# Optimization experiments

Measured on AMD Instinct MI355X. Metric: run time of the kernel, lower is better.

The kernel has to match this reference:

```python
import jax, jax.numpy as jnp
import numpy as np

WEIGHT = 0.1
NEIGHBORHOOD_SIZE = 3
EPSILON = 1e-06


def setup_inputs() -> dict:
    key = jax.random.key(0)
    x = jax.random.normal(key, (8, 3, 1024, 1024), dtype=jnp.float32)
    return {"x": x}


def reference(x):
    b, c, h, w = x.shape
    total = jnp.zeros((), dtype=x.dtype)
    for k in range(-NEIGHBORHOOD_SIZE, NEIGHBORHOOD_SIZE + 1):
        for l in range(-NEIGHBORHOOD_SIZE, NEIGHBORHOOD_SIZE + 1):
            if k == 0 and l == 0:
                continue
            shifted = jnp.roll(x, shift=(k, l), axis=(2, 3))
            diff = jnp.abs(x - shifted)
            total = total + jnp.sqrt(diff * diff + EPSILON).sum()
    return WEIGHT * total / (b * c * h * w)
```

## Files before the change

### kernel.cpp

```cpp
#include <hip/hip_runtime.h>


#define HDIM 1024
#define WDIM 1024
#define PLANES 24
#define MASK 1023
#define NTOT (PLANES * HDIM * WDIM)
#define RROWS 16
#define BLOCKS_PER_PLANE (HDIM / RROWS)
#define NBLOCKS (PLANES * BLOCKS_PER_PLANE)

__device__ __forceinline__ void load_row(const float* __restrict__ rb,
                                         int j, int cl, int cr, float* w) {
    float4 a = *(const float4*)(rb + cl);
    float4 b = *(const float4*)(rb + j);
    float4 c = *(const float4*)(rb + cr);
    w[0] = a.x; w[1] = a.y; w[2]  = a.z; w[3]  = a.w;
    w[4] = b.x; w[5] = b.y; w[6]  = b.z; w[7]  = b.w;
    w[8] = c.x; w[9] = c.y; w[10] = c.z; w[11] = c.w;
}

__global__ __launch_bounds__(256) void btv_main(const float* __restrict__ x,
                                                float* __restrict__ partial) {
    const int plane  = blockIdx.x / BLOCKS_PER_PLANE;
    const int istart = (blockIdx.x % BLOCKS_PER_PLANE) * RROWS;
    const int j  = threadIdx.x << 2;
    const int cl = (j - 4) & MASK;
    const int cr = (j + 4) & MASK;
    const float* pbase = x + (size_t)plane * (HDIM * WDIM);

    float buf[RROWS + 3][12];

#pragma unroll
    for (int m = 0; m < 6; ++m)
        load_row(pbase + (((istart + m) & MASK) * WDIM), j, cl, cr, buf[m]);

    float acc0 = 0.f, acc1 = 0.f, acc2 = 0.f, acc3 = 0.f;

#pragma unroll
    for (int r = 0; r < RROWS; ++r) {
        if (r + 6 <= RROWS + 2)
            load_row(pbase + (((istart + r + 6) & MASK) * WDIM), j, cl, cr,
                     buf[r + 6]);

        const float* w0 = buf[r];
        const float* w1 = buf[r + 1];
        const float* w2 = buf[r + 2];
        const float* w3 = buf[r + 3];

#pragma unroll
        for (int p = 0; p < 4; ++p) {
            const float own = w0[4 + p];
            float a = 0.f;
            a += fabsf(own - w0[5 + p]);
            a += fabsf(own - w0[6 + p]);
            a += fabsf(own - w0[7 + p]);
#pragma unroll
            for (int l = -3; l <= 3; ++l) a += fabsf(own - w1[4 + p + l]);
#pragma unroll
            for (int l = -3; l <= 3; ++l) a += fabsf(own - w2[4 + p + l]);
#pragma unroll
            for (int l = -3; l <= 3; ++l) a += fabsf(own - w3[4 + p + l]);
            if (p == 0) acc0 += a;
            else if (p == 1) acc1 += a;
            else if (p == 2) acc2 += a;
            else acc3 += a;
        }
    }

    float acc = (acc0 + acc1) + (acc2 + acc3);

#pragma unroll
    for (int off = 32; off > 0; off >>= 1)
        acc += __shfl_down(acc, off, 64);

    __shared__ float s[4];
    const int lane = threadIdx.x & 63;
    const int wid  = threadIdx.x >> 6;
    if (lane == 0) s[wid] = acc;
    __syncthreads();
    if (threadIdx.x == 0)
        partial[blockIdx.x] = (s[0] + s[1]) + (s[2] + s[3]);
}

__global__ __launch_bounds__(256) void btv_fin(const float* __restrict__ partial,
                                               float* __restrict__ out) {
    double s = 0.0;
    for (int i = threadIdx.x; i < NBLOCKS; i += 256)
        s += (double)partial[i];
#pragma unroll
    for (int off = 32; off > 0; off >>= 1)
        s += __shfl_down(s, off, 64);
    __shared__ double sh[4];
    const int lane = threadIdx.x & 63;
    const int wid  = threadIdx.x >> 6;
    if (lane == 0) sh[wid] = s;
    __syncthreads();
    if (threadIdx.x == 0) {
        double t = (sh[0] + sh[1]) + (sh[2] + sh[3]);
        *out = (float)(t * (0.2 / (double)NTOT));
    }
}

extern "C" void kernel_launch(void* const* d_in, const int* in_sizes, int n_in,
                              void* d_out, int out_size, void* d_ws, size_t ws_size,
                              hipStream_t stream) {
    const float* x = (const float*)d_in[0];
    float* out = (float*)d_out;
    float* partial = (float*)d_ws;

    btv_main<<<NBLOCKS, 256, 0, stream>>>(x, partial);
    btv_fin<<<1, 256, 0, stream>>>(partial, out);
}
```

Before: 150.6 us.

## Use rolling 8-slot register ring buffer with 32 rows per block

Replaces the fully unrolled per-block row buffer with an 8-slot circular register buffer of float4 rows. This allows 32 rows per block, halving the redundant halo row reloads, and adds a launch-bounds occupancy hint. Loads of the next row are issued one iteration ahead inside a partially unrolled outer loop. It halves the block count and may add register pressure or reduce the prefetch distance compared to the earlier six-row lookahead.

```diff
diff --git a/kernel.cpp b/kernel.cpp
--- a/kernel.cpp
+++ b/kernel.cpp
@@ -6,22 +6,16 @@
 #define PLANES 24
 #define MASK 1023
 #define NTOT (PLANES * HDIM * WDIM)
-#define RROWS 16
+#define RROWS 32
 #define BLOCKS_PER_PLANE (HDIM / RROWS)
 #define NBLOCKS (PLANES * BLOCKS_PER_PLANE)
 
-__device__ __forceinline__ void load_row(const float* __restrict__ rb,
-                                         int j, int cl, int cr, float* w) {
-    float4 a = *(const float4*)(rb + cl);
-    float4 b = *(const float4*)(rb + j);
-    float4 c = *(const float4*)(rb + cr);
-    w[0] = a.x; w[1] = a.y; w[2]  = a.z; w[3]  = a.w;
-    w[4] = b.x; w[5] = b.y; w[6]  = b.z; w[7]  = b.w;
-    w[8] = c.x; w[9] = c.y; w[10] = c.z; w[11] = c.w;
+__device__ __forceinline__ float getc(const float4 v, int c) {
+    return c == 0 ? v.x : (c == 1 ? v.y : (c == 2 ? v.z : v.w));
 }
 
-__global__ __launch_bounds__(256) void btv_main(const float* __restrict__ x,
-                                                float* __restrict__ partial) {
+__global__ __launch_bounds__(256, 3) void btv_main(const float* __restrict__ x,
+                                                   float* __restrict__ partial) {
     const int plane  = blockIdx.x / BLOCKS_PER_PLANE;
     const int istart = (blockIdx.x % BLOCKS_PER_PLANE) * RROWS;
     const int j  = threadIdx.x << 2;
@@ -29,55 +23,69 @@
     const int cr = (j + 4) & MASK;
     const float* pbase = x + (size_t)plane * (HDIM * WDIM);
 
-    float buf[RROWS + 3][12];
+    float4 buf[8][3];
+
+#define LOAD_ROW(slot, m) do {                                          \
+        const float* rb_ = pbase + (((istart + (m)) & MASK) * WDIM);    \
+        buf[slot][0] = *(const float4*)(rb_ + cl);                      \
+        buf[slot][1] = *(const float4*)(rb_ + j);                       \
+        buf[slot][2] = *(const float4*)(rb_ + cr);                      \
+    } while (0)
+
+#define WV(s, c) getc(buf[s][(c) >> 2], (c) & 3)
+
+#define COMPUTE(rr) do {                                                \
+        const int s0 = (rr) & 7, s1 = ((rr) + 1) & 7,                   \
+                  s2 = ((rr) + 2) & 7, s3 = ((rr) + 3) & 7;             \
+        _Pragma("unroll")                                               \
+        for (int p = 0; p < 4; ++p) {                                   \
+            const float own = WV(s0, 4 + p);                            \
+            float a = fabsf(own - WV(s0, 5 + p));                       \
+            a += fabsf(own - WV(s0, 6 + p));                            \
+            a += fabsf(own - WV(s0, 7 + p));                            \
+            _Pragma("unroll")                                           \
+            for (int l = -3; l <= 3; ++l) a += fabsf(own - WV(s1, 4 + p + l)); \
+            _Pragma("unroll")                                           \
+            for (int l = -3; l <= 3; ++l) a += fabsf(own - WV(s2, 4 + p + l)); \
+            _Pragma("unroll")                                           \
+            for (int l = -3; l <= 3; ++l) a += fabsf(own - WV(s3, 4 + p + l)); \
+            acc[p] += a;                                                \
+        }                                                               \
+    } while (0)
 
 #pragma unroll
-    for (int m = 0; m < 6; ++m)
-        load_row(pbase + (((istart + m) & MASK) * WDIM), j, cl, cr, buf[m]);
+    for (int m = 0; m < 7; ++m) LOAD_ROW(m & 7, m);
 
-    float acc0 = 0.f, acc1 = 0.f, acc2 = 0.f, acc3 = 0.f;
+    float acc[4] = {0.f, 0.f, 0.f, 0.f};
 
+    for (int ro = 0; ro < 3; ++ro) {
+        const int rbase = ro << 3;
 #pragma unroll
-    for (int r = 0; r < RROWS; ++r) {
-        if (r + 6 <= RROWS + 2)
-            load_row(pbase + (((istart + r + 6) & MASK) * WDIM), j, cl, cr,
-                     buf[r + 6]);
-
-        const float* w0 = buf[r];
-        const float* w1 = buf[r + 1];
-        const float* w2 = buf[r + 2];
-        const float* w3 = buf[r + 3];
-
-#pragma unroll
-        for (int p = 0; p < 4; ++p) {
-            const float own = w0[4 + p];
-            float a = 0.f;
-            a += fabsf(own - w0[5 + p]);
-            a += fabsf(own - w0[6 + p]);
-            a += fabsf(own - w0[7 + p]);
-#pragma unroll
-            for (int l = -3; l <= 3; ++l) a += fabsf(own - w1[4 + p + l]);
-#pragma unroll
-            for (int l = -3; l <= 3; ++l) a += fabsf(own - w2[4 + p + l]);
-#pragma unroll
-            for (int l = -3; l <= 3; ++l) a += fabsf(own - w3[4 + p + l]);
-            if (p == 0) acc0 += a;
-            else if (p == 1) acc1 += a;
-            else if (p == 2) acc2 += a;
-            else acc3 += a;
+        for (int rr = 0; rr < 8; ++rr) {
+            LOAD_ROW((rr + 7) & 7, rbase + rr + 7);
+            COMPUTE(rr);
         }
     }
+#pragma unroll
+    for (int rr = 0; rr < 8; ++rr) {
+        if (rr < 4) LOAD_ROW((rr + 7) & 7, 24 + rr + 7);
+        COMPUTE(rr);
+    }
 
-    float acc = (acc0 + acc1) + (acc2 + acc3);
+#undef LOAD_ROW
+#undef WV
+#undef COMPUTE
+
+    float acct = (acc[0] + acc[1]) + (acc[2] + acc[3]);
 
 #pragma unroll
     for (int off = 32; off > 0; off >>= 1)
-        acc += __shfl_down(acc, off, 64);
+        acct += __shfl_down(acct, off, 64);
 
     __shared__ float s[4];
     const int lane = threadIdx.x & 63;
     const int wid  = threadIdx.x >> 6;
-    if (lane == 0) s[wid] = acc;
+    if (lane == 0) s[wid] = acct;
     __syncthreads();
     if (threadIdx.x == 0)
         partial[blockIdx.x] = (s[0] + s[1]) + (s[2] + s[3]);
```

Result: slower. 275.6 us (+83.1%).
